# Kernel tuning notes

Hardware: AMD Instinct MI355X
Metric: run time of the kernel (lower is better)

Reference implementation:

```python
import jax, jax.numpy as jnp
import numpy as np

N_NODES = 100_000
N_EDGES = 6_400_000
CH = 5


def setup_inputs() -> dict:
    key = jax.random.key(0)
    ks = jax.random.split(key, 16)
    inp = {
        "x": jax.random.normal(ks[0], (N_NODES, 2), dtype=jnp.float32),
        "edge_index": jax.random.randint(ks[1], (2, N_EDGES), 0, N_NODES, dtype=jnp.int64 if jax.config.jax_enable_x64 else jnp.int32).astype(jnp.int32),
        "edge_attr": jax.random.uniform(ks[2], (N_EDGES, 1), dtype=jnp.float32),
        "lin1_w": jax.random.normal(ks[3], (2, CH), dtype=jnp.float32) * 0.5,
        "lin1_b": jax.random.normal(ks[4], (CH,), dtype=jnp.float32) * 0.1,
        "conv1_wf": jax.random.normal(ks[5], (2 * CH + 1, CH), dtype=jnp.float32) * 0.3,
        "conv1_bf": jax.random.normal(ks[6], (CH,), dtype=jnp.float32) * 0.1,
        "conv1_ws": jax.random.normal(ks[7], (2 * CH + 1, CH), dtype=jnp.float32) * 0.3,
        "conv1_bs": jax.random.normal(ks[8], (CH,), dtype=jnp.float32) * 0.1,
        "conv2_wf": jax.random.normal(ks[9], (2 * CH + 1, CH), dtype=jnp.float32) * 0.3,
        "conv2_bf": jax.random.normal(ks[10], (CH,), dtype=jnp.float32) * 0.1,
        "conv2_ws": jax.random.normal(ks[11], (2 * CH + 1, CH), dtype=jnp.float32) * 0.3,
        "conv2_bs": jax.random.normal(ks[12], (CH,), dtype=jnp.float32) * 0.1,
        "lin2_w": jax.random.normal(ks[13], (CH, 2), dtype=jnp.float32) * 0.5,
        "lin2_b": jax.random.normal(ks[14], (2,), dtype=jnp.float32) * 0.1,
    }
    return inp


def cgconv(x, edge_index, edge_attr, wf, bf, ws, bs):
    # PyG CGConv: x_i' = x_i + sum_{j->i} sigmoid(z W_f + b_f) * softplus(z W_s + b_s)
    # z = [x_i, x_j, e_ij]; edge_index[0]=source j, edge_index[1]=target i
    src, dst = edge_index[0], edge_index[1]
    z = jnp.concatenate([x[dst], x[src], edge_attr], axis=-1)  # [E, 2C+dim]
    msg = jax.nn.sigmoid(z @ wf + bf) * jax.nn.softplus(z @ ws + bs)  # [E, C]
    agg = jax.ops.segment_sum(msg, dst, num_segments=x.shape[0])  # [N, C]
    return x + agg


def reference(x, edge_index, edge_attr,
              lin1_w, lin1_b,
              conv1_wf, conv1_bf, conv1_ws, conv1_bs,
              conv2_wf, conv2_bf, conv2_ws, conv2_bs,
              lin2_w, lin2_b):
    h = x @ lin1_w + lin1_b  # [N, C]
    h = cgconv(h, edge_index, edge_attr, conv1_wf, conv1_bf, conv1_ws, conv1_bs)
    h = cgconv(h, edge_index, edge_attr, conv2_wf, conv2_bf, conv2_ws, conv2_bs)
    return h @ lin2_w + lin2_b  # [N, 2]
```

## Files before the change

### kernel.cpp

```cpp
#include <hip/hip_runtime.h>
#include <hip/hip_fp16.h>

constexpr int NN = 100000;
constexpr int NE = 6400000;
constexpr int BSH = 7;
constexpr int BN = 1 << BSH;
constexpr int NBUCK = (NN + BN - 1) / BN;
constexpr int BCAP = 9216;
constexpr int STILE = 8192;
constexpr int NSB = (NE + STILE - 1) / STILE;
constexpr int NP = 1024;

#define LOG2E 1.44269504f
#define LN2   0.69314718f


__global__ __launch_bounds__(256) void k_lin2(const float* __restrict__ h,
                                              const float* __restrict__ w,
                                              const float* __restrict__ b,
                                              float* __restrict__ out) {
    int n = blockIdx.x * 256 + threadIdx.x;
    if (n >= NN) return;
    float o0 = b[0], o1 = b[1];
#pragma unroll
    for (int c = 0; c < 5; ++c) {
        float hv = h[(size_t)n * 5 + c];
        o0 += hv * w[2 * c];
        o1 += hv * w[2 * c + 1];
    }
    out[2 * n] = o0;
    out[2 * n + 1] = o1;
}

__device__ __forceinline__ void prep_core(const float hv[5],
                                          const float* __restrict__ wf,
                                          const float* __restrict__ bf,
                                          const float* __restrict__ ws,
                                          const float* __restrict__ bs,
                                          int n, float* __restrict__ TD,
                                          unsigned short* __restrict__ TSh) {
    float tg[5], ts[5], sg[5], ss[5];
#pragma unroll
    for (int c = 0; c < 5; ++c) {
        float a = bf[c], d = bs[c], u = 0.f, v = 0.f;
#pragma unroll
        for (int k = 0; k < 5; ++k) {
            a += hv[k] * wf[k * 5 + c];
            d += hv[k] * ws[k * 5 + c];
            u += hv[k] * wf[(5 + k) * 5 + c];
            v += hv[k] * ws[(5 + k) * 5 + c];
        }
        tg[c] = a * LOG2E; ts[c] = d * LOG2E;
        sg[c] = u * LOG2E; ss[c] = v * LOG2E;
    }
    float4* Dp = (float4*)(TD + (size_t)n * 12);
    Dp[0] = make_float4(tg[0], tg[1], tg[2], tg[3]);
    Dp[1] = make_float4(tg[4], ts[0], ts[1], ts[2]);
    Dp[2] = make_float4(ts[3], ts[4], 0.f, 0.f);

    unsigned short r[10];
#pragma unroll
    for (int c = 0; c < 5; ++c) {
        r[c]     = __half_as_ushort(__float2half_rn(sg[c]));
        r[5 + c] = __half_as_ushort(__float2half_rn(ss[c]));
    }
    uint4 w0, w1;
    w0.x = (unsigned)r[0] | ((unsigned)r[1] << 16);
    w0.y = (unsigned)r[2] | ((unsigned)r[3] << 16);
    w0.z = (unsigned)r[4] | ((unsigned)r[5] << 16);
    w0.w = (unsigned)r[6] | ((unsigned)r[7] << 16);
    w1.x = (unsigned)r[8] | ((unsigned)r[9] << 16);
    w1.y = 0; w1.z = 0; w1.w = 0;
    *(uint4*)(TSh + (size_t)n * 16) = w0;
    *(uint4*)(TSh + (size_t)n * 16 + 8) = w1;
}

__global__ __launch_bounds__(256) void k_prep1(const float* __restrict__ x,
                                               const float* __restrict__ l1w,
                                               const float* __restrict__ l1b,
                                               const float* __restrict__ wf,
                                               const float* __restrict__ bf,
                                               const float* __restrict__ ws,
                                               const float* __restrict__ bs,
                                               float* __restrict__ TD,
                                               unsigned short* __restrict__ TSh,
                                               float* __restrict__ h) {
    int n = blockIdx.x * 256 + threadIdx.x;
    if (n >= NN) return;
    float x0 = x[2 * n], x1 = x[2 * n + 1];
    float hv[5];
#pragma unroll
    for (int c = 0; c < 5; ++c) {
        hv[c] = l1b[c] + x0 * l1w[c] + x1 * l1w[5 + c];
        h[(size_t)n * 5 + c] = hv[c];
    }
    prep_core(hv, wf, bf, ws, bs, n, TD, TSh);
}

__global__ __launch_bounds__(256) void k_prep(const float* __restrict__ h,
                                              const float* __restrict__ wf,
                                              const float* __restrict__ bf,
                                              const float* __restrict__ ws,
                                              const float* __restrict__ bs,
                                              float* __restrict__ TD,
                                              unsigned short* __restrict__ TSh) {
    int n = blockIdx.x * 256 + threadIdx.x;
    if (n >= NN) return;
    float hv[5];
#pragma unroll
    for (int k = 0; k < 5; ++k) hv[k] = h[(size_t)n * 5 + k];
    prep_core(hv, wf, bf, ws, bs, n, TD, TSh);
}

__global__ __launch_bounds__(256) void k_initcurs(int* __restrict__ gcurs) {
    int i = blockIdx.x * 256 + threadIdx.x;
    if (i < NBUCK) gcurs[i] = i * BCAP;
}

__global__ __launch_bounds__(512) void k_scatter4(const int* __restrict__ ei,
                                                  const float* __restrict__ ea,
                                                  int* __restrict__ gcurs,
                                                  unsigned int* __restrict__ rec) {
    __shared__ unsigned int lrec[STILE];
    __shared__ unsigned int spk[STILE];
    __shared__ int C[NBUCK];
    __shared__ int loc[NBUCK];
    __shared__ int gbase[NBUCK];
    __shared__ int A[NP];
    const int tid = threadIdx.x, blk = blockIdx.x;
    const int base = blk * STILE;
    const int m = min(STILE, NE - base);

    for (int i = tid; i < NBUCK; i += 512) C[i] = 0;
    __syncthreads();

    const int m4 = m >> 2;
    const int4* s4 = (const int4*)(ei + base);
    const int4* d4 = (const int4*)(ei + NE + base);
    const float4* a4 = (const float4*)(ea + base);
    for (int q = tid; q < m4; q += 512) {
        int4 s = s4[q];
        int4 d = d4[q];
        float4 a = a4[q];
        int k = q * 4;
        lrec[k + 0] = (unsigned)s.x | ((unsigned)(d.x & (BN - 1)) << 17) |
                      (__float2uint_rn(a.x * 255.f) << 24);
        lrec[k + 1] = (unsigned)s.y | ((unsigned)(d.y & (BN - 1)) << 17) |
                      (__float2uint_rn(a.y * 255.f) << 24);
        lrec[k + 2] = (unsigned)s.z | ((unsigned)(d.z & (BN - 1)) << 17) |
                      (__float2uint_rn(a.z * 255.f) << 24);
        lrec[k + 3] = (unsigned)s.w | ((unsigned)(d.w & (BN - 1)) << 17) |
                      (__float2uint_rn(a.w * 255.f) << 24);
        atomicAdd(&C[(unsigned)d.x >> BSH], 1);
        atomicAdd(&C[(unsigned)d.y >> BSH], 1);
        atomicAdd(&C[(unsigned)d.z >> BSH], 1);
        atomicAdd(&C[(unsigned)d.w >> BSH], 1);
    }
    __syncthreads();

    for (int b = tid; b < NBUCK; b += 512)
        gbase[b] = C[b] ? atomicAdd(&gcurs[b], C[b]) : 0;
    for (int i = tid; i < NP; i += 512) A[i] = (i < NBUCK) ? C[i] : 0;
    __syncthreads();

    for (int d = 1; d < NP; d <<= 1) {
        int i = (tid + 1) * (d << 1) - 1;
        if (i < NP) A[i] += A[i - d];
        __syncthreads();
    }
    if (tid == 0) A[NP - 1] = 0;
    __syncthreads();
    for (int d = NP >> 1; d >= 1; d >>= 1) {
        int i = (tid + 1) * (d << 1) - 1;
        if (i < NP) { int t = A[i - d]; A[i - d] = A[i]; A[i] += t; }
        __syncthreads();
    }
    for (int b = tid; b < NBUCK; b += 512) loc[b] = A[b];
    __syncthreads();

    for (int k = tid; k < m; k += 512) {
        int bkt = (unsigned)ei[NE + base + k] >> BSH;
        int p = atomicAdd(&loc[bkt], 1);
        spk[p] = (unsigned)k | ((unsigned)bkt << 16);
    }
    __syncthreads();

    for (int p = tid; p < m; p += 512) {
        unsigned pk = spk[p];
        int k = pk & 0xFFFF;
        int bkt = pk >> 16;
        rec[gbase[bkt] + (p - A[bkt])] = lrec[k];
    }
}

__global__ __launch_bounds__(512) void k_sortbkt(const int* __restrict__ gcurs,
                                                 unsigned int* __restrict__ rec,
                                                 int2* __restrict__ nrange) {
    __shared__ unsigned int lrec[BCAP];
    __shared__ int cnt[BN];
    __shared__ int curs[BN];
    const int b = blockIdx.x, tid = threadIdx.x;
    const int e0 = b * BCAP;
    const int m = gcurs[b] - e0;
    const int node0 = b << BSH;
    const int nloc = min(BN, NN - node0);

    for (int i = tid; i < m; i += 512) lrec[i] = rec[e0 + i];
    if (tid < BN) cnt[tid] = 0;
    __syncthreads();
    for (int i = tid; i < m; i += 512)
        atomicAdd(&cnt[(lrec[i] >> 17) & (BN - 1)], 1);
    __syncthreads();
    int v = (tid < BN) ? cnt[tid] : 0;
    for (int off = 1; off < BN; off <<= 1) {
        int t = 0;
        if (tid < BN && tid >= off) t = cnt[tid - off];
        __syncthreads();
        if (tid < BN) cnt[tid] += t;
        __syncthreads();
    }
    if (tid < BN) {
        int excl = cnt[tid] - v;
        curs[tid] = excl;
        if (tid < nloc)
            nrange[node0 + tid] = make_int2(e0 + excl, e0 + excl + v);
    }
    __syncthreads();
    for (int i = tid; i < m; i += 512) {
        unsigned int r = lrec[i];
        int dl = (r >> 17) & (BN - 1);
        int pos = atomicAdd(&curs[dl], 1);
        rec[e0 + pos] = r;
    }
}

__global__ __launch_bounds__(256) void k_conv_csr(
        const unsigned int* __restrict__ rec, const int2* __restrict__ nrange,
        const float* __restrict__ TD, const unsigned short* __restrict__ TSh,
        const float* __restrict__ wf, const float* __restrict__ ws,
        float* __restrict__ h ) {
    const int tid = threadIdx.x;
    const int lane = tid & 15;
    const int n = blockIdx.x * 16 + (tid >> 4);

    float WFE[5], WSE[5];
#pragma unroll
    for (int c = 0; c < 5; ++c) {
        WFE[c] = wf[50 + c] * LOG2E;
        WSE[c] = ws[50 + c] * LOG2E;
    }

    const float4* Dp = (const float4*)(TD + (size_t)n * 12);
    float4 d0 = Dp[0], d1 = Dp[1], d2 = Dp[2];
    const float Tg[5] = {d0.x, d0.y, d0.z, d0.w, d1.x};
    const float Ts[5] = {d1.y, d1.z, d1.w, d2.x, d2.y};

    float acc[5] = {0.f, 0.f, 0.f, 0.f, 0.f};
    const int2 rg = nrange[n];
    const int eEnd = rg.y;
    for (int e = rg.x + lane; e < eEnd; e += 64) {
        unsigned r[4];
        bool vld[4];
        float4 q0[4];
        unsigned q1[4];
        float av[4];
#pragma unroll
        for (int j = 0; j < 4; ++j) {
            int ej = e + j * 16;
            vld[j] = ej < eEnd;
            r[j] = rec[vld[j] ? ej : e];
        }
#pragma unroll
        for (int j = 0; j < 4; ++j) {
            const unsigned src = r[j] & 0x1FFFFu;
            const unsigned short* row = TSh + (size_t)src * 16;
            q0[j] = *(const float4*)row;
            q1[j] = *(const unsigned*)(row + 8);
            av[j] = (float)(r[j] >> 24) * (1.f / 255.f);
        }
#pragma unroll
        for (int j = 0; j < 4; ++j) {
            if (!vld[j]) continue;
            union { float4 f; __half2 h2[4]; } u; u.f = q0[j];
            float2 p0 = __half22float2(u.h2[0]);
            float2 p1 = __half22float2(u.h2[1]);
            float2 p2 = __half22float2(u.h2[2]);
            float2 p3 = __half22float2(u.h2[3]);
            __half2 h4 = *(__half2*)&q1[j];
            float2 p4 = __half22float2(h4);
            const float Sg[5] = {p0.x, p0.y, p1.x, p1.y, p2.x};
            const float Ss[5] = {p2.y, p3.x, p3.y, p4.x, p4.y};
            const float a = av[j];
#pragma unroll
            for (int c = 0; c < 5; ++c) {
                const float f = Tg[c] + Sg[c] + a * WFE[c];
                const float s = Ts[c] + Ss[c] + a * WSE[c];
                const float t = exp2f(-f);
                const float sig = __builtin_amdgcn_rcpf(1.f + t);
                const float uu = exp2f(-fabsf(s));
                const float sp = log2f(1.f + uu) + fmaxf(s, 0.f);
                acc[c] = fmaf(sig, sp, acc[c]);
            }
        }
    }
#pragma unroll
    for (int off = 8; off >= 1; off >>= 1)
#pragma unroll
        for (int c = 0; c < 5; ++c)
            acc[c] += __shfl_xor(acc[c], off, 16);
    if (lane == 0) {
#pragma unroll
        for (int c = 0; c < 5; ++c)
            h[(size_t)n * 5 + c] += LN2 * acc[c];
    }
}

__global__ __launch_bounds__(256) void k_prep_fb(const float* __restrict__ h,
                                                 const float* __restrict__ wf,
                                                 const float* __restrict__ bf,
                                                 const float* __restrict__ ws,
                                                 const float* __restrict__ bs,
                                                 float* __restrict__ T,
                                                 float* __restrict__ S,
                                                 float* __restrict__ hout) {
    int n = blockIdx.x * 256 + threadIdx.x;
    if (n >= NN) return;
    float hv[5];
#pragma unroll
    for (int k = 0; k < 5; ++k) hv[k] = h[5 * n + k];
    float tf[5], ts[5], sf[5], ss[5];
#pragma unroll
    for (int c = 0; c < 5; ++c) {
        float a = bf[c], d = bs[c], u = 0.f, v = 0.f;
#pragma unroll
        for (int k = 0; k < 5; ++k) {
            a += hv[k] * wf[k * 5 + c];
            d += hv[k] * ws[k * 5 + c];
            u += hv[k] * wf[(5 + k) * 5 + c];
            v += hv[k] * ws[(5 + k) * 5 + c];
        }
        tf[c] = a; ts[c] = d; sf[c] = u; ss[c] = v;
    }
    float4* Tp = (float4*)(T + (size_t)n * 16);
    Tp[0] = make_float4(tf[0], tf[1], tf[2], tf[3]);
    Tp[1] = make_float4(tf[4], ts[0], ts[1], ts[2]);
    Tp[2] = make_float4(ts[3], ts[4], 0.f, 0.f);
    float4* Sp = (float4*)(S + (size_t)n * 16);
    Sp[0] = make_float4(sf[0], sf[1], sf[2], sf[3]);
    Sp[1] = make_float4(sf[4], ss[0], ss[1], ss[2]);
    Sp[2] = make_float4(ss[3], ss[4], 0.f, 0.f);
#pragma unroll
    for (int c = 0; c < 5; ++c) hout[5 * n + c] = hv[c];
}

__global__ __launch_bounds__(256) void k_conv_atomic(const int* __restrict__ ei,
                                                     const float* __restrict__ ea,
                                                     const float* __restrict__ T,
                                                     const float* __restrict__ S,
                                                     const float* __restrict__ wf,
                                                     const float* __restrict__ ws,
                                                     float* __restrict__ hout) {
    int e = blockIdx.x * 256 + threadIdx.x;
    if (e >= NE) return;
    int src = ei[e];
    int dst = ei[NE + e];
    float a = ea[e];
    const float4* Tp = (const float4*)(T + (size_t)dst * 16);
    const float4* Sp = (const float4*)(S + (size_t)src * 16);
    float4 t0 = Tp[0], t1 = Tp[1], t2 = Tp[2];
    float4 s0 = Sp[0], s1 = Sp[1], s2 = Sp[2];
    float za[5] = {t0.x + s0.x, t0.y + s0.y, t0.z + s0.z, t0.w + s0.w, t1.x + s1.x};
    float zs[5] = {t1.y + s1.y, t1.z + s1.z, t1.w + s1.w, t2.x + s2.x, t2.y + s2.y};
    float* outp = hout + (size_t)dst * 5;
#pragma unroll
    for (int c = 0; c < 5; ++c) {
        float f = za[c] + a * wf[50 + c];
        float s = zs[c] + a * ws[50 + c];
        float sig = 1.f / (1.f + __expf(-f));
        float sp = __logf(1.f + __expf(-fabsf(s))) + fmaxf(s, 0.f);
        unsafeAtomicAdd(outp + c, sig * sp);
    }
}

__global__ __launch_bounds__(256) void k_lin1_fb(const float* __restrict__ x,
                                                 const float* __restrict__ w,
                                                 const float* __restrict__ b,
                                                 float* __restrict__ h) {
    int n = blockIdx.x * 256 + threadIdx.x;
    if (n >= NN) return;
    float x0 = x[2 * n], x1 = x[2 * n + 1];
#pragma unroll
    for (int c = 0; c < 5; ++c)
        h[5 * n + c] = b[c] + x0 * w[c] + x1 * w[5 + c];
}

extern "C" void kernel_launch(void* const* d_in, const int* in_sizes, int n_in,
                              void* d_out, int out_size, void* d_ws, size_t ws_size,
                              hipStream_t stream) {
    const float* x    = (const float*)d_in[0];
    const int*   ei   = (const int*)d_in[1];
    const float* ea   = (const float*)d_in[2];
    const float* l1w  = (const float*)d_in[3];
    const float* l1b  = (const float*)d_in[4];
    const float* c1wf = (const float*)d_in[5];
    const float* c1bf = (const float*)d_in[6];
    const float* c1ws = (const float*)d_in[7];
    const float* c1bs = (const float*)d_in[8];
    const float* c2wf = (const float*)d_in[9];
    const float* c2bf = (const float*)d_in[10];
    const float* c2ws = (const float*)d_in[11];
    const float* c2bs = (const float*)d_in[12];
    const float* l2w  = (const float*)d_in[13];
    const float* l2b  = (const float*)d_in[14];
    float* out = (float*)d_out;
    char* ws = (char*)d_ws;

    size_t o_rec    = 0;
    size_t o_nrange = o_rec + (size_t)NBUCK * BCAP * 4;
    size_t o_gcurs  = o_nrange + (size_t)NN * 8;
    size_t o_TD     = (o_gcurs + (size_t)NBUCK * 4 + 15) & ~(size_t)15;
    size_t o_TS     = o_TD + (size_t)NN * 12 * 4;
    size_t o_h      = o_TS + (size_t)NN * 16 * 2;
    size_t need     = o_h + (size_t)NN * 5 * 4;

    int nb_n = (NN + 255) / 256;

    if (ws_size >= need) {
        unsigned int* rec    = (unsigned int*)(ws + o_rec);
        int2* nrange         = (int2*)(ws + o_nrange);
        int* gcurs           = (int*)(ws + o_gcurs);
        float* TD            = (float*)(ws + o_TD);
        unsigned short* TSh  = (unsigned short*)(ws + o_TS);
        float* h             = (float*)(ws + o_h);

        k_initcurs<<<(NBUCK + 255) / 256, 256, 0, stream>>>(gcurs);
        k_scatter4<<<NSB,   512, 0, stream>>>(ei, ea, gcurs, rec);
        k_sortbkt <<<NBUCK, 512, 0, stream>>>(gcurs, rec, nrange);

        k_prep1<<<nb_n, 256, 0, stream>>>(x, l1w, l1b,
                                          c1wf, c1bf, c1ws, c1bs, TD, TSh, h);
        k_conv_csr<<<NN / 16, 256, 0, stream>>>(rec, nrange, TD, TSh,
                                                c1wf, c1ws, h);
        k_prep<<<nb_n, 256, 0, stream>>>(h, c2wf, c2bf, c2ws, c2bs, TD, TSh);
        k_conv_csr<<<NN / 16, 256, 0, stream>>>(rec, nrange, TD, TSh,
                                                c2wf, c2ws, h);
        k_lin2<<<nb_n, 256, 0, stream>>>(h, l2w, l2b, out);
    } else {
        float* h0 = (float*)(ws);
        float* h1 = (float*)(ws + 2000000);
        float* h2 = h0;
        float* T  = (float*)(ws + 4000000);
        float* S  = (float*)(ws + 10400000);
        int nb_e = (NE + 255) / 256;

        k_lin1_fb<<<nb_n, 256, 0, stream>>>(x, l1w, l1b, h0);
        k_prep_fb<<<nb_n, 256, 0, stream>>>(h0, c1wf, c1bf, c1ws, c1bs, T, S, h1);
        k_conv_atomic<<<nb_e, 256, 0, stream>>>(ei, ea, T, S, c1wf, c1ws, h1);
        k_prep_fb<<<nb_n, 256, 0, stream>>>(h1, c2wf, c2bf, c2ws, c2bs, T, S, h2);
        k_conv_atomic<<<nb_e, 256, 0, stream>>>(ei, ea, T, S, c2wf, c2ws, h2);
        k_lin2<<<nb_n, 256, 0, stream>>>(h2, l2w, l2b, out);
    }
}
```

Measured before the change: 196.8 us.

## Compute edge messages in packed fp16 and pad bucket cursors apart

Moves the per-edge sigmoid/softplus message math in the gather kernel from fp32 to packed half2 arithmetic. Gate and softplus pre-activations are negated and paired so one h2exp2 covers both, and the edge-weight term becomes a half2 FMA. Node-side tables now store the negated values interleaved as half2 pairs. Bucket cursors used by the scatter atomics are spaced 16 ints apart to avoid contention on shared cache lines. The fp16 math lowers ALU and transcendental cost per edge but risks accuracy loss, and the cursor array grows 16x.

```diff
diff --git a/kernel.cpp b/kernel.cpp
--- a/kernel.cpp
+++ b/kernel.cpp
@@ -10,6 +10,7 @@
 constexpr int STILE = 8192;
 constexpr int NSB = (NE + STILE - 1) / STILE;
 constexpr int NP = 1024;
+constexpr int GS = 16;
 
 #define LOG2E 1.44269504f
 #define LN2   0.69314718f
@@ -50,27 +51,23 @@
             u += hv[k] * wf[(5 + k) * 5 + c];
             v += hv[k] * ws[(5 + k) * 5 + c];
         }
-        tg[c] = a * LOG2E; ts[c] = d * LOG2E;
-        sg[c] = u * LOG2E; ss[c] = v * LOG2E;
+        tg[c] = -a * LOG2E; ts[c] = -d * LOG2E;
+        sg[c] = -u * LOG2E; ss[c] = -v * LOG2E;
     }
     float4* Dp = (float4*)(TD + (size_t)n * 12);
     Dp[0] = make_float4(tg[0], tg[1], tg[2], tg[3]);
     Dp[1] = make_float4(tg[4], ts[0], ts[1], ts[2]);
     Dp[2] = make_float4(ts[3], ts[4], 0.f, 0.f);
 
-    unsigned short r[10];
-#pragma unroll
-    for (int c = 0; c < 5; ++c) {
-        r[c]     = __half_as_ushort(__float2half_rn(sg[c]));
-        r[5 + c] = __half_as_ushort(__float2half_rn(ss[c]));
-    }
-    uint4 w0, w1;
-    w0.x = (unsigned)r[0] | ((unsigned)r[1] << 16);
-    w0.y = (unsigned)r[2] | ((unsigned)r[3] << 16);
-    w0.z = (unsigned)r[4] | ((unsigned)r[5] << 16);
-    w0.w = (unsigned)r[6] | ((unsigned)r[7] << 16);
-    w1.x = (unsigned)r[8] | ((unsigned)r[9] << 16);
-    w1.y = 0; w1.z = 0; w1.w = 0;
+    unsigned p[5];
+#pragma unroll
+    for (int c = 0; c < 5; ++c) {
+        unsigned lo = (unsigned)__half_as_ushort(__float2half_rn(sg[c]));
+        unsigned hi = (unsigned)__half_as_ushort(__float2half_rn(ss[c]));
+        p[c] = lo | (hi << 16);
+    }
+    uint4 w0 = make_uint4(p[0], p[1], p[2], p[3]);
+    uint4 w1 = make_uint4(p[4], 0u, 0u, 0u);
     *(uint4*)(TSh + (size_t)n * 16) = w0;
     *(uint4*)(TSh + (size_t)n * 16 + 8) = w1;
 }
@@ -114,7 +111,7 @@
 
 __global__ __launch_bounds__(256) void k_initcurs(int* __restrict__ gcurs) {
     int i = blockIdx.x * 256 + threadIdx.x;
-    if (i < NBUCK) gcurs[i] = i * BCAP;
+    if (i < NBUCK) gcurs[(size_t)i * GS] = i * BCAP;
 }
 
 __global__ __launch_bounds__(512) void k_scatter4(const int* __restrict__ ei,
@@ -159,7 +156,7 @@
     __syncthreads();
 
     for (int b = tid; b < NBUCK; b += 512)
-        gbase[b] = C[b] ? atomicAdd(&gcurs[b], C[b]) : 0;
+        gbase[b] = C[b] ? atomicAdd(&gcurs[(size_t)b * GS], C[b]) : 0;
     for (int i = tid; i < NP; i += 512) A[i] = (i < NBUCK) ? C[i] : 0;
     __syncthreads();
 
@@ -201,7 +198,7 @@
     __shared__ int curs[BN];
     const int b = blockIdx.x, tid = threadIdx.x;
     const int e0 = b * BCAP;
-    const int m = gcurs[b] - e0;
+    const int m = gcurs[(size_t)b * GS] - e0;
     const int node0 = b << BSH;
     const int nloc = min(BN, NN - node0);
 
@@ -243,17 +240,21 @@
     const int lane = tid & 15;
     const int n = blockIdx.x * 16 + (tid >> 4);
 
-    float WFE[5], WSE[5];
-#pragma unroll
-    for (int c = 0; c < 5; ++c) {
-        WFE[c] = wf[50 + c] * LOG2E;
-        WSE[c] = ws[50 + c] * LOG2E;
-    }
+    __half2 we2[5];
+#pragma unroll
+    for (int c = 0; c < 5; ++c)
+        we2[c] = __floats2half2_rn(-wf[50 + c] * LOG2E, -ws[50 + c] * LOG2E);
 
     const float4* Dp = (const float4*)(TD + (size_t)n * 12);
     float4 d0 = Dp[0], d1 = Dp[1], d2 = Dp[2];
     const float Tg[5] = {d0.x, d0.y, d0.z, d0.w, d1.x};
     const float Ts[5] = {d1.y, d1.z, d1.w, d2.x, d2.y};
+    __half2 dd2[5];
+#pragma unroll
+    for (int c = 0; c < 5; ++c) dd2[c] = __floats2half2_rn(Tg[c], Ts[c]);
+
+    const __half2 one2 = __float2half2_rn(1.f);
+    const __half hz = __float2half(0.f);
 
     float acc[5] = {0.f, 0.f, 0.f, 0.f, 0.f};
     const int2 rg = nrange[n];
@@ -263,7 +264,7 @@
         bool vld[4];
         float4 q0[4];
         unsigned q1[4];
-        float av[4];
+        __half2 a2[4];
 #pragma unroll
         for (int j = 0; j < 4; ++j) {
             int ej = e + j * 16;
@@ -276,30 +277,26 @@
             const unsigned short* row = TSh + (size_t)src * 16;
             q0[j] = *(const float4*)row;
             q1[j] = *(const unsigned*)(row + 8);
-            av[j] = (float)(r[j] >> 24) * (1.f / 255.f);
+            a2[j] = __float2half2_rn((float)(r[j] >> 24) * (1.f / 255.f));
         }
 #pragma unroll
         for (int j = 0; j < 4; ++j) {
             if (!vld[j]) continue;
             union { float4 f; __half2 h2[4]; } u; u.f = q0[j];
-            float2 p0 = __half22float2(u.h2[0]);
-            float2 p1 = __half22float2(u.h2[1]);
-            float2 p2 = __half22float2(u.h2[2]);
-            float2 p3 = __half22float2(u.h2[3]);
-            __half2 h4 = *(__half2*)&q1[j];
-            float2 p4 = __half22float2(h4);
-            const float Sg[5] = {p0.x, p0.y, p1.x, p1.y, p2.x};
-            const float Ss[5] = {p2.y, p3.x, p3.y, p4.x, p4.y};
-            const float a = av[j];
+            __half2 s2[5] = {u.h2[0], u.h2[1], u.h2[2], u.h2[3],
+                             *(__half2*)&q1[j]};
 #pragma unroll
             for (int c = 0; c < 5; ++c) {
-                const float f = Tg[c] + Sg[c] + a * WFE[c];
-                const float s = Ts[c] + Ss[c] + a * WSE[c];
-                const float t = exp2f(-f);
-                const float sig = __builtin_amdgcn_rcpf(1.f + t);
-                const float uu = exp2f(-fabsf(s));
-                const float sp = log2f(1.f + uu) + fmaxf(s, 0.f);
-                acc[c] = fmaf(sig, sp, acc[c]);
+                __half2 z2 = __hadd2(__hfma2(a2[j], we2[c], dd2[c]), s2[c]);
+                __half zx = __low2half(z2);
+                __half zy = __high2half(z2);
+                __half nab = __hmin(zy, __hneg(zy));
+                __half2 e2 = h2exp2(__halves2half2(zx, nab));
+                __half2 o2 = __hadd2(e2, one2);
+                float sig = __half2float(hrcp(__low2half(o2)));
+                float lg  = __half2float(hlog2(__high2half(o2)));
+                float mx  = __half2float(__hmin(zy, hz));
+                acc[c] = fmaf(sig, lg - mx, acc[c]);
             }
         }
     }
@@ -418,7 +415,7 @@
     size_t o_rec    = 0;
     size_t o_nrange = o_rec + (size_t)NBUCK * BCAP * 4;
     size_t o_gcurs  = o_nrange + (size_t)NN * 8;
-    size_t o_TD     = (o_gcurs + (size_t)NBUCK * 4 + 15) & ~(size_t)15;
+    size_t o_TD     = (o_gcurs + (size_t)NBUCK * GS * 4 + 15) & ~(size_t)15;
     size_t o_TS     = o_TD + (size_t)NN * 12 * 4;
     size_t o_h      = o_TS + (size_t)NN * 16 * 2;
     size_t need     = o_h + (size_t)NN * 5 * 4;
```

Measured after the change: 210.3 us. 6.9% more time.
